# Kernel tuning notes

Hardware: AMD Instinct MI355X
Metric: run time of the kernel (lower is better)

Reference implementation:

```python
import jax, jax.numpy as jnp
import numpy as np

TEMPERATURE = 0.5


def setup_inputs() -> dict:
    key = jax.random.key(0)
    k1, k2 = jax.random.split(key)
    B, C, H, W = 64, 256, 32, 32
    inputs = jax.random.normal(k1, (B, C, H, W), dtype=jnp.float32)
    targets = jax.random.normal(k2, (B, C, H, W), dtype=jnp.float32)
    return {"inputs": inputs, "targets": targets}


def reference(inputs, targets):
    # [B, C, H, W] -> [H, W, B, C]
    x = jnp.transpose(inputs, (2, 3, 0, 1))
    y = jnp.transpose(targets, (2, 3, 0, 1))
    B = x.shape[-2]
    feats = jnp.concatenate([x, y], axis=-2)  # [H, W, 2B, C]
    eps = jnp.finfo(feats.dtype).eps
    # cosine similarity: normalize each vector with eps-clamped norm, then dot
    norms = jnp.maximum(jnp.linalg.norm(feats, axis=-1, keepdims=True), eps)
    fn = feats / norms
    sim = jnp.einsum('hwic,hwjc->hwij', fn, fn)  # [H, W, 2B, 2B]
    # mask self-similarity diagonal with -inf
    mask = jnp.eye(2 * B, dtype=bool)
    sim = jnp.where(mask, -jnp.inf, sim)
    log_sm = jax.nn.log_softmax(sim / TEMPERATURE, axis=-1)
    pos = jnp.concatenate(
        [jnp.diagonal(log_sm, offset=B, axis1=-2, axis2=-1),
         jnp.diagonal(log_sm, offset=-B, axis1=-2, axis2=-1)],
        axis=-1,
    )  # [H, W, 2B]
    return -jnp.mean(pos)
```

## Files before the change

### kernel.cpp

```cpp
#include <hip/hip_runtime.h>
#include <stdint.h>

#define HWPOS 1024
#define CCH   256
#define RROWS 128
#define EPSF  1.1920928955078125e-07f

typedef __attribute__((ext_vector_type(4))) float float4v;

__device__ float g_acc[64 * 16];

__device__ __forceinline__ uint32_t pk4_fp8(float a, float b, float c, float d) {
  int v = 0;
  v = __builtin_amdgcn_cvt_pk_fp8_f32(a, b, v, false);
  v = __builtin_amdgcn_cvt_pk_fp8_f32(c, d, v, true);
  return (uint32_t)v;
}


__global__ __launch_bounds__(256, 4) void k_transpose(const float* __restrict__ inp,
                                                      const float* __restrict__ tgt,
                                                      unsigned char* __restrict__ wsF,
                                                      int r0) {
  __shared__ uint4 Ls[1024];
  const int t    = threadIdx.x;
  const int hq   = t & 31;
  const int ddl  = t >> 5;
  const int bx   = blockIdx.x;
  const int r    = r0 + blockIdx.y;
  const int half = blockIdx.z;
  if (r0 == 0 && bx == 0 && blockIdx.y == 0 && half == 0 && t < 64)
    g_acc[t * 16] = 0.0f;
  const int dd = half * 8 + ddl;
  const float* src = (r < 64) ? (inp + (size_t)r * CCH * HWPOS)
                              : (tgt + (size_t)(r - 64) * CCH * HWPOS);
  const float* p = src + (size_t)(dd * 16) * HWPOS + bx * 128 + hq * 4;
  float4 v[16];
#pragma unroll
  for (int e = 0; e < 16; ++e) v[e] = *(const float4*)(p + (size_t)e * HWPOS);
  const int sbase = ddl ^ (hq & 7);
#pragma unroll
  for (int q = 0; q < 4; ++q) {
    float x[16];
#pragma unroll
    for (int e = 0; e < 16; ++e)
      x[e] = (q == 0) ? v[e].x : (q == 1) ? v[e].y : (q == 2) ? v[e].z : v[e].w;
    uint4 o;
    o.x = pk4_fp8(x[0],  x[1],  x[2],  x[3]);
    o.y = pk4_fp8(x[4],  x[5],  x[6],  x[7]);
    o.z = pk4_fp8(x[8],  x[9],  x[10], x[11]);
    o.w = pk4_fp8(x[12], x[13], x[14], x[15]);
    Ls[(hq * 4 + q) * 8 + sbase] = o;
  }
  __syncthreads();
  const int sl = t & 7;
  const int hb = t >> 3;
  const int mh = r & 7;
  const int half_out = half ^ ((r >> 3) & 1);
  const int ddn = sl ^ mh;
  const size_t gbase = (size_t)r * 262144 + (size_t)(bx * 128) * 256
                     + (size_t)(half_out * 128 + sl * 16);
#pragma unroll
  for (int j = 0; j < 4; ++j) {
    const int hwl = hb + 32 * j;
    uint4 d = Ls[hwl * 8 + (ddn ^ ((hwl >> 2) & 7))];
    *(uint4*)(wsF + gbase + (size_t)hwl * 256) = d;
  }
}

__global__ __launch_bounds__(512, 4) void k_gram(const unsigned char* __restrict__ wsF) {
  __shared__ unsigned char Fs[32768];
  __shared__ float sInv[RROWS];
  __shared__ float wred[8];
  const int t  = threadIdx.x;
  const int hw = blockIdx.x;
  const int lane = t & 63;
  const int w    = t >> 6;
  const int lid  = lane & 15;
  const int quad = lane >> 4;
  float4v acc[8];
#pragma unroll
  for (int ni = 0; ni < 8; ++ni) acc[ni] = (float4v){0.f, 0.f, 0.f, 0.f};
#pragma unroll
  for (int it = 0; it < 4; ++it) {
    const int ch = it * 512 + t;
    const size_t goff = (size_t)(ch >> 4) * 262144
                      + (size_t)hw * 256
                      + (size_t)(ch & 15) * 16;
    __builtin_amdgcn_global_load_lds(
        (const __attribute__((address_space(1))) unsigned int*)(wsF + goff),
        (__attribute__((address_space(3))) unsigned int*)(Fs + (size_t)ch * 16),
        16, 0, 0);
  }
  __syncthreads();
  const int rowA = (w << 4) | lid;
#pragma unroll
  for (int ks = 0; ks < 8; ++ks) {
    const int d    = 2 * ks + (quad >> 1);
    const int off  = ((d ^ lid) << 4) + (quad & 1) * 8;
    long a = *(const long*)&Fs[rowA * 256 + off];
#pragma unroll
    for (int ni = 0; ni < 8; ++ni) {
      long b = *(const long*)&Fs[(((ni << 4) | lid)) * 256 + off];
      acc[ni] = __builtin_amdgcn_mfma_f32_16x16x32_fp8_fp8(a, b, acc[ni], 0, 0, 0);
    }
  }
  {
    float diagv = 0.f;
#pragma unroll
    for (int ni = 0; ni < 8; ++ni) {
      if (ni == w) {
#pragma unroll
        for (int e = 0; e < 4; ++e)
          if (e == (lid & 3)) diagv = acc[ni][e];
      }
    }
    if ((lid >> 2) == quad) {
      sInv[(w << 4) | lid] = 1.0f / fmaxf(sqrtf(diagv), EPSF);
    }
  }
  __syncthreads();
  float invj[8];
#pragma unroll
  for (int ni = 0; ni < 8; ++ni) invj[ni] = sInv[(ni << 4) | lid];
  const int tj = (w + 4) & 7;
  float lacc = 0.f;
#pragma unroll
  for (int reg = 0; reg < 4; ++reg) {
    const int rloc = quad * 4 + reg;
    const int rg   = (w << 4) | rloc;
    const float invi = sInv[rg];
    float v[8];
#pragma unroll
    for (int ni = 0; ni < 8; ++ni) v[ni] = 2.0f * acc[ni][reg] * invi * invj[ni];
#pragma unroll
    for (int ni = 0; ni < 8; ++ni)
      if (ni == w && lid == rloc) v[ni] = -3.0e38f;
    float mx = v[0];
#pragma unroll
    for (int ni = 1; ni < 8; ++ni) mx = fmaxf(mx, v[ni]);
#pragma unroll
    for (int sh = 1; sh < 16; sh <<= 1) mx = fmaxf(mx, __shfl_xor(mx, sh, 16));
    float sm = 0.f;
#pragma unroll
    for (int ni = 0; ni < 8; ++ni) sm += __expf(v[ni] - mx);
#pragma unroll
    for (int sh = 1; sh < 16; sh <<= 1) sm += __shfl_xor(sm, sh, 16);
    const float lse = mx + __logf(sm);
    float cand = 0.f;
#pragma unroll
    for (int ni = 0; ni < 8; ++ni)
      if (ni == tj) cand = v[ni];
    const float vp = __shfl(cand, rloc, 16);
    lacc += vp - lse;
  }
#pragma unroll
  for (int sh = 1; sh < 64; sh <<= 1) lacc += __shfl_xor(lacc, sh, 64);
  if (lane == 0) wred[w] = lacc;
  __syncthreads();
  if (t == 0) {
    float tot = 0.f;
#pragma unroll
    for (int i = 0; i < 8; ++i) tot += wred[i];
    atomicAdd(&g_acc[(hw & 63) * 16], tot);
  }
}

__global__ __launch_bounds__(64) void k_reduce(float* __restrict__ out) {
  const int t = threadIdx.x;
  float v = g_acc[t * 16];
#pragma unroll
  for (int sh = 1; sh < 64; sh <<= 1) v += __shfl_xor(v, sh, 64);
  if (t == 0) out[0] = -v * (1.0f / 2097152.0f);
}

extern "C" void kernel_launch(void* const* d_in, const int* in_sizes, int n_in,
                              void* d_out, int out_size, void* d_ws, size_t ws_size,
                              hipStream_t stream) {
  const float* inp = (const float*)d_in[0];
  const float* tgt = (const float*)d_in[1];
  unsigned char* wsF = (unsigned char*)d_ws;
  k_transpose<<<dim3(8, 64, 2), 256, 0, stream>>>(inp, tgt, wsF, 0);
  k_transpose<<<dim3(8, 64, 2), 256, 0, stream>>>(inp, tgt, wsF, 64);
  k_gram<<<dim3(HWPOS), 512, 0, stream>>>(wsF);
  k_reduce<<<1, 64, 0, stream>>>((float*)d_out);
}
```

Baseline: 174.7 us.

## Restructure transpose into single launch with new fp8 workspace layout

The two transpose launches become one. Each block handles one row and a quarter of the channels, staging fp32 tiles in 64KB of LDS over four 16-channel steps before packing to fp8. The workspace layout moves to 64-byte chunks per (row, channel-quarter, hw), and the gram kernel's load addressing is updated to match. This is meant to remove a launch, lengthen the contiguous global reads, and change the write pattern. In exchange, the large LDS footprint and the extra syncs per step lower occupancy.

```diff
diff --git a/kernel.cpp b/kernel.cpp
--- a/kernel.cpp
+++ b/kernel.cpp
@@ -18,53 +18,46 @@
 }
 
 
-__global__ __launch_bounds__(256, 4) void k_transpose(const float* __restrict__ inp,
+__global__ __launch_bounds__(512, 2) void k_transpose(const float* __restrict__ inp,
                                                       const float* __restrict__ tgt,
-                                                      unsigned char* __restrict__ wsF,
-                                                      int r0) {
-  __shared__ uint4 Ls[1024];
-  const int t    = threadIdx.x;
-  const int hq   = t & 31;
-  const int ddl  = t >> 5;
-  const int bx   = blockIdx.x;
-  const int r    = r0 + blockIdx.y;
-  const int half = blockIdx.z;
-  if (r0 == 0 && bx == 0 && blockIdx.y == 0 && half == 0 && t < 64)
-    g_acc[t * 16] = 0.0f;
-  const int dd = half * 8 + ddl;
+                                                      unsigned char* __restrict__ wsF) {
+  __shared__ float T[16 * 1024];
+  const int t = threadIdx.x;
+  const int r = blockIdx.x;
+  const int q = blockIdx.y;
+  if (r == 0 && q == 0 && t < 64) g_acc[t * 16] = 0.0f;
   const float* src = (r < 64) ? (inp + (size_t)r * CCH * HWPOS)
                               : (tgt + (size_t)(r - 64) * CCH * HWPOS);
-  const float* p = src + (size_t)(dd * 16) * HWPOS + bx * 128 + hq * 4;
-  float4 v[16];
+  const int c_l = t >> 5;
+  const int l32 = t & 31;
+  const int qs  = q ^ ((r >> 2) & 3);
+  const size_t regbase = (size_t)(r * 4 + qs) * 65536;
 #pragma unroll
-  for (int e = 0; e < 16; ++e) v[e] = *(const float4*)(p + (size_t)e * HWPOS);
-  const int sbase = ddl ^ (hq & 7);
+  for (int k = 0; k < 4; ++k) {
+    const int dd = q * 4 + k;
+    const float* gp = src + (size_t)(dd * 16 + c_l) * HWPOS + l32 * 4;
+    float4 v[8];
 #pragma unroll
-  for (int q = 0; q < 4; ++q) {
-    float x[16];
+    for (int j = 0; j < 8; ++j) v[j] = *(const float4*)(gp + j * 128);
 #pragma unroll
-    for (int e = 0; e < 16; ++e)
-      x[e] = (q == 0) ? v[e].x : (q == 1) ? v[e].y : (q == 2) ? v[e].z : v[e].w;
-    uint4 o;
-    o.x = pk4_fp8(x[0],  x[1],  x[2],  x[3]);
-    o.y = pk4_fp8(x[4],  x[5],  x[6],  x[7]);
-    o.z = pk4_fp8(x[8],  x[9],  x[10], x[11]);
-    o.w = pk4_fp8(x[12], x[13], x[14], x[15]);
-    Ls[(hq * 4 + q) * 8 + sbase] = o;
-  }
-  __syncthreads();
-  const int sl = t & 7;
-  const int hb = t >> 3;
-  const int mh = r & 7;
-  const int half_out = half ^ ((r >> 3) & 1);
-  const int ddn = sl ^ mh;
-  const size_t gbase = (size_t)r * 262144 + (size_t)(bx * 128) * 256
-                     + (size_t)(half_out * 128 + sl * 16);
+    for (int j = 0; j < 8; ++j)
+      *(float4*)&T[c_l * 1024 + l32 * 4 + j * 128] = v[j];
+    __syncthreads();
+    const int sl3 = k ^ (r & 3);
 #pragma unroll
-  for (int j = 0; j < 4; ++j) {
-    const int hwl = hb + 32 * j;
-    uint4 d = Ls[hwl * 8 + (ddn ^ ((hwl >> 2) & 7))];
-    *(uint4*)(wsF + gbase + (size_t)hwl * 256) = d;
+    for (int h2 = 0; h2 < 2; ++h2) {
+      const int hw = t + h2 * 512;
+      float x[16];
+#pragma unroll
+      for (int c = 0; c < 16; ++c) x[c] = T[c * 1024 + hw];
+      uint4 o;
+      o.x = pk4_fp8(x[0],  x[1],  x[2],  x[3]);
+      o.y = pk4_fp8(x[4],  x[5],  x[6],  x[7]);
+      o.z = pk4_fp8(x[8],  x[9],  x[10], x[11]);
+      o.w = pk4_fp8(x[12], x[13], x[14], x[15]);
+      *(uint4*)(wsF + regbase + (size_t)hw * 64 + sl3 * 16) = o;
+    }
+    __syncthreads();
   }
 }
 
@@ -84,9 +77,10 @@
 #pragma unroll
   for (int it = 0; it < 4; ++it) {
     const int ch = it * 512 + t;
-    const size_t goff = (size_t)(ch >> 4) * 262144
-                      + (size_t)hw * 256
-                      + (size_t)(ch & 15) * 16;
+    const int rr = ch >> 4;
+    const int ss = ch & 15;
+    const size_t goff = (size_t)((rr << 2) + (ss >> 2)) * 65536
+                      + (size_t)hw * 64 + (size_t)(ss & 3) * 16;
     __builtin_amdgcn_global_load_lds(
         (const __attribute__((address_space(1))) unsigned int*)(wsF + goff),
         (__attribute__((address_space(3))) unsigned int*)(Fs + (size_t)ch * 16),
@@ -180,8 +174,7 @@
   const float* inp = (const float*)d_in[0];
   const float* tgt = (const float*)d_in[1];
   unsigned char* wsF = (unsigned char*)d_ws;
-  k_transpose<<<dim3(8, 64, 2), 256, 0, stream>>>(inp, tgt, wsF, 0);
-  k_transpose<<<dim3(8, 64, 2), 256, 0, stream>>>(inp, tgt, wsF, 64);
+  k_transpose<<<dim3(128, 4), 512, 0, stream>>>(inp, tgt, wsF);
   k_gram<<<dim3(HWPOS), 512, 0, stream>>>(wsF);
   k_reduce<<<1, 64, 0, stream>>>((float*)d_out);
 }
```

Result: slower. 178.4 us (+2.1%).
